# Kernel optimization log

Measured on AMD Instinct MI355X. Metric: run time of the kernel, lower is better.

The kernel has to match this reference:

```python
import jax, jax.numpy as jnp
import numpy as np

GAMMA = 0.95        # gamma_lemma: persistence decay per cycle (eq. 12.1)
KAPPA = 0.1         # kappa_interfere: lateral interference strength (eq. 12.3)
T_STEPS = 50        # t_lemma_steps: integration window before selection (eq. 12.2)
FLOOR = 1e-6        # confidence_floor for peak-to-average ratio

B, N_CONCEPTS, N_LEMMAS = 4096, 1024, 512


def setup_inputs() -> dict:
    key = jax.random.key(0)
    k1, k2 = jax.random.split(key, 2)
    # kernel boundary hands in a normalized concept distribution
    c_raw = jax.random.uniform(k1, (B, N_CONCEPTS), dtype=jnp.float32)
    c_lex = c_raw / jnp.sum(c_raw, axis=-1, keepdims=True)
    # TiedSubstrate W_C_to_L: (out_dim=n_lemmas, in_dim=n_concepts)
    W = jax.random.normal(k2, (N_LEMMAS, N_CONCEPTS), dtype=jnp.float32) / np.sqrt(N_CONCEPTS)
    # persistent lemma activation buffer a_lemma, zero at reset
    a0 = jnp.zeros((B, N_LEMMAS), dtype=jnp.float32)
    return {"c_lex": c_lex, "W": W, "a0": a0}


def reference(c_lex, W, a0):
    """Integrate lemma activations for T_STEPS cycles, then select.

    Per cycle (eq. 12.1 + 12.3):
      a <- gamma * a + c_lex @ W^T            # decay + concept->lemma drive
      a <- a - kappa * (sum_j a_j - a)        # lateral interference from other lemmas
      a <- max(a, 0)                          # rectify activations
    Selection (eq. 12.2): argmax over lemmas; confidence = peak / max(mean, floor).
    """
    def step(a, _):
        a = GAMMA * a + jnp.einsum('bc,lc->bl', c_lex, W)   # (B, n_lemmas)
        a = a - KAPPA * (jnp.sum(a, axis=-1, keepdims=True) - a)
        a = jnp.maximum(a, 0.0)
        return a, None

    a, _ = jax.lax.scan(step, a0, None, length=T_STEPS)
    peak = jnp.max(a, axis=-1)
    mean = jnp.mean(a, axis=-1)
    confidence = peak / jnp.maximum(mean, FLOOR)
    selected = jnp.argmax(a, axis=-1)
    return a, selected, confidence
```

## Files before the change

### kernel.cpp

```cpp
#include <hip/hip_runtime.h>
#include <hip/hip_bf16.h>

#define BATCH 4096
#define NC    1024
#define NL    512
#define TSTEPS 50
#define GAMMA_C 0.95f
#define KAPPA_C 0.1f
#define FLOOR_C 1e-6f

typedef __attribute__((ext_vector_type(8))) short short8;
typedef __attribute__((ext_vector_type(4))) float f32x4;

__device__ __forceinline__ void split2_pk(float x0, float x1,
                                          unsigned& hp, unsigned& lp) {
    union { __hip_bfloat162 b; unsigned u; } ch, cl;
    ch.b = __float22bfloat162_rn(make_float2(x0, x1));
    hp = ch.u;
    const float hf0 = __uint_as_float(hp << 16);
    const float hf1 = __uint_as_float(hp & 0xFFFF0000u);
    cl.b = __float22bfloat162_rn(make_float2(x0 - hf0, x1 - hf1));
    lp = cl.u;
}

#define W_FLOATS (NL * NC)
#define W_BLOCKS (W_FLOATS / (256 * 8))
#define A_BLOCKS ((BATCH * NC) / (256 * 8))

__global__ __launch_bounds__(256)
void convert_hilo(const float* __restrict__ W, const float* __restrict__ A,
                  unsigned short* __restrict__ Whi, unsigned short* __restrict__ Wlo,
                  unsigned short* __restrict__ Ahi, unsigned short* __restrict__ Alo) {
    const int b = blockIdx.x;
    const float* src;
    unsigned short *dh, *dl;
    if (b < W_BLOCKS) {
        const size_t fidx = ((size_t)b * 256 + threadIdx.x) * 8;
        src = W + fidx; dh = Whi + fidx; dl = Wlo + fidx;
    } else {
        const size_t fidx = ((size_t)(b - W_BLOCKS) * 256 + threadIdx.x) * 8;
        src = A + fidx; dh = Ahi + fidx; dl = Alo + fidx;
    }
    const float4 v0 = ((const float4*)src)[0];
    const float4 v1 = ((const float4*)src)[1];
    uint4 h, l;
    split2_pk(v0.x, v0.y, h.x, l.x);
    split2_pk(v0.z, v0.w, h.y, l.y);
    split2_pk(v1.x, v1.y, h.z, l.z);
    split2_pk(v1.z, v1.w, h.w, l.w);
    *(uint4*)dh = h;
    *(uint4*)dl = l;
}

__device__ __forceinline__ float wave_sum_bcast(float x) {
    float f = x;
    f += __int_as_float(__builtin_amdgcn_update_dpp(
            0, __float_as_int(f), 0x111, 0xf, 0xf, true));
    f += __int_as_float(__builtin_amdgcn_update_dpp(
            0, __float_as_int(f), 0x112, 0xf, 0xf, true));
    f += __int_as_float(__builtin_amdgcn_update_dpp(
            0, __float_as_int(f), 0x114, 0xf, 0xf, true));
    f += __int_as_float(__builtin_amdgcn_update_dpp(
            0, __float_as_int(f), 0x118, 0xf, 0xf, true));
    f += __int_as_float(__builtin_amdgcn_update_dpp(
            0, __float_as_int(f), 0x142, 0xa, 0xf, true));
    f += __int_as_float(__builtin_amdgcn_update_dpp(
            0, __float_as_int(f), 0x143, 0xc, 0xf, true));
    return __int_as_float(__builtin_amdgcn_readlane(__float_as_int(f), 63));
}

__device__ __forceinline__ void glds16(const unsigned short* g, unsigned short* l) {
    __builtin_amdgcn_global_load_lds(
        (__attribute__((address_space(1))) void*)(g),
        (__attribute__((address_space(3))) void*)(l), 16, 0, 0);
}

#define TM 128
#define TN 128
#define GK 32
#define SPLITK 4
#define NST (NC / SPLITK / GK)

__global__ __launch_bounds__(256)
void gemm_bf16x2(const unsigned short* __restrict__ Ahi, const unsigned short* __restrict__ Alo,
                 const unsigned short* __restrict__ Whi, const unsigned short* __restrict__ Wlo,
                 float* __restrict__ Dp) {
    __shared__ unsigned short S[2][4][TM * GK];

    const int tid  = threadIdx.x;
    const int lane = tid & 63;
    const int w    = tid >> 6;

    const int b    = blockIdx.x;
    const int xcd  = b & 7;
    const int slot = b >> 3;
    const int mi_b = xcd * 4 + (slot & 3);
    const int nk   = slot >> 2;
    const int ni_b = nk & 3;
    const int kz   = nk >> 2;

    const int m0 = mi_b * TM;
    const int n0 = ni_b * TN;
    const int kb = kz * (NC / SPLITK);

    const int srow = w * 32 + (lane >> 2);
    const int scol = (lane & 3) * 8;
    const unsigned short* gAh = Ahi + (size_t)(m0 + srow) * NC + kb + scol;
    const unsigned short* gAl = Alo + (size_t)(m0 + srow) * NC + kb + scol;
    const unsigned short* gBh = Whi + (size_t)(n0 + srow) * NC + kb + scol;
    const unsigned short* gBl = Wlo + (size_t)(n0 + srow) * NC + kb + scol;
    const int ld0 = (w * 32) * GK + lane * 8;

    const int mw   = (w >> 1) * 64;
    const int nw   = (w & 1) * 64;
    const int sr   = lane & 15;
    const int quad = lane >> 4;
    const int rA = (mw + sr) * GK + quad * 8;
    const int rB = (nw + sr) * GK + quad * 8;

    f32x4 acc[4][4];
    #pragma unroll
    for (int i = 0; i < 4; ++i)
        #pragma unroll
        for (int j = 0; j < 4; ++j)
            acc[i][j] = (f32x4){0.f, 0.f, 0.f, 0.f};

    #define STAGE(buf, kofs)                                          \
        {                                                             \
            const int ko = (kofs);                                    \
            glds16(gAh + ko,           &S[buf][0][ld0]);              \
            glds16(gAh + ko + 16 * NC, &S[buf][0][ld0 + 16 * GK]);    \
            glds16(gAl + ko,           &S[buf][1][ld0]);              \
            glds16(gAl + ko + 16 * NC, &S[buf][1][ld0 + 16 * GK]);    \
            glds16(gBh + ko,           &S[buf][2][ld0]);              \
            glds16(gBh + ko + 16 * NC, &S[buf][2][ld0 + 16 * GK]);    \
            glds16(gBl + ko,           &S[buf][3][ld0]);              \
            glds16(gBl + ko + 16 * NC, &S[buf][3][ld0 + 16 * GK]);    \
        }

    #define KSTEP(CUR, VMSTR, DO_STAGE, NEXTK)                                 \
        {                                                                      \
            asm volatile("s_waitcnt vmcnt(" VMSTR ")" ::: "memory");           \
            __builtin_amdgcn_sched_barrier(0);                                 \
            __builtin_amdgcn_s_barrier();                                      \
            __builtin_amdgcn_sched_barrier(0);                                 \
            short8 afh[4], afl[4], bfh[4], bfl[4];                             \
            _Pragma("unroll")                                                  \
            for (int mi = 0; mi < 4; ++mi) {                                   \
                afh[mi] = *(const short8*)&S[CUR][0][rA + mi * 16 * GK];       \
                afl[mi] = *(const short8*)&S[CUR][1][rA + mi * 16 * GK];       \
            }                                                                  \
            _Pragma("unroll")                                                  \
            for (int ni = 0; ni < 4; ++ni) {                                   \
                bfh[ni] = *(const short8*)&S[CUR][2][rB + ni * 16 * GK];       \
                bfl[ni] = *(const short8*)&S[CUR][3][rB + ni * 16 * GK];       \
            }                                                                  \
            _Pragma("unroll")                                                  \
            for (int mi = 0; mi < 4; ++mi) {                                   \
                _Pragma("unroll")                                              \
                for (int ni = 0; ni < 4; ++ni) {                               \
                    acc[mi][ni] = __builtin_amdgcn_mfma_f32_16x16x32_bf16(     \
                        afh[mi], bfh[ni], acc[mi][ni], 0, 0, 0);               \
                    acc[mi][ni] = __builtin_amdgcn_mfma_f32_16x16x32_bf16(     \
                        afh[mi], bfl[ni], acc[mi][ni], 0, 0, 0);               \
                    acc[mi][ni] = __builtin_amdgcn_mfma_f32_16x16x32_bf16(     \
                        afl[mi], bfh[ni], acc[mi][ni], 0, 0, 0);               \
                }                                                              \
            }                                                                  \
            __builtin_amdgcn_sched_barrier(0);                                 \
            __builtin_amdgcn_s_barrier();                                      \
            __builtin_amdgcn_sched_barrier(0);                                 \
            if (DO_STAGE) STAGE(CUR, NEXTK);                                   \
        }

    STAGE(0, 0);
    STAGE(1, GK);

    #pragma unroll 2
    for (int s = 0; s < NST - 2; ++s)
        KSTEP((s & 1), "8", true, (s + 2) * GK);
    KSTEP(0, "8", false, 0);
    KSTEP(1, "0", false, 0);

    float* Dz = Dp + (size_t)kz * BATCH * NL;
    #pragma unroll
    for (int mi = 0; mi < 4; ++mi) {
        #pragma unroll
        for (int ni = 0; ni < 4; ++ni) {
            const int col = n0 + nw + ni * 16 + sr;
            #pragma unroll
            for (int r = 0; r < 4; ++r) {
                const int row = m0 + mw + mi * 16 + quad * 4 + r;
                Dz[(size_t)row * NL + col] = acc[mi][ni][r];
            }
        }
    }
}

template<int SK>
__global__ __launch_bounds__(256)
void iterate_select(const float* __restrict__ Dp,
                    float* __restrict__ a_out,
                    float* __restrict__ sel_out, float* __restrict__ conf_out) {
    const int lane = threadIdx.x & 63;
    const int wave = threadIdx.x >> 6;
    const int row  = blockIdx.x * 4 + wave;

    float d[8];
    {
        float4 v[SK][2];
        #pragma unroll
        for (int s = 0; s < SK; ++s) {
            const float4* ps = (const float4*)(Dp + (size_t)s * BATCH * NL
                                               + (size_t)row * NL + lane * 8);
            v[s][0] = ps[0];
            v[s][1] = ps[1];
        }
        d[0] = v[0][0].x; d[1] = v[0][0].y; d[2] = v[0][0].z; d[3] = v[0][0].w;
        d[4] = v[0][1].x; d[5] = v[0][1].y; d[6] = v[0][1].z; d[7] = v[0][1].w;
        #pragma unroll
        for (int s = 1; s < SK; ++s) {
            d[0] += v[s][0].x; d[1] += v[s][0].y; d[2] += v[s][0].z; d[3] += v[s][0].w;
            d[4] += v[s][1].x; d[5] += v[s][1].y; d[6] += v[s][1].z; d[7] += v[s][1].w;
        }
    }

    float a[8];
    #pragma unroll
    for (int j = 0; j < 8; ++j) a[j] = 0.f;

    const float K1 = 1.0f + KAPPA_C;

    for (int t = 0; t < TSTEPS; ++t) {
        #pragma unroll
        for (int j = 0; j < 8; ++j) a[j] = fmaf(GAMMA_C, a[j], d[j]);

        float t4a = a[0] + a[4], t4b = a[1] + a[5], t4c = a[2] + a[6], t4d = a[3] + a[7];
        float t2a = t4a + t4c, t2b = t4b + t4d;
        const float S = wave_sum_bcast(t2a + t2b);

        const float h = -KAPPA_C * S;
        #pragma unroll
        for (int j = 0; j < 8; ++j) {
            const float v = fmaf(K1, a[j], h);
            a[j] = v > 0.f ? v : 0.f;
        }
    }

    float m4a = fmaxf(a[0], a[4]), m4b = fmaxf(a[1], a[5]);
    float m4c = fmaxf(a[2], a[6]), m4d = fmaxf(a[3], a[7]);
    float peak = fmaxf(fmaxf(m4a, m4b), fmaxf(m4c, m4d));
    float s4a = a[0] + a[4], s4b = a[1] + a[5], s4c = a[2] + a[6], s4d = a[3] + a[7];
    float ssum = wave_sum_bcast((s4a + s4b) + (s4c + s4d));

    #pragma unroll
    for (int m = 1; m < 64; m <<= 1)
        peak = fmaxf(peak, __shfl_xor(peak, m, 64));

    const float mean = ssum * (1.0f / (float)NL);
    const float conf = peak / fmaxf(mean, FLOOR_C);

    int idx = 0x7fffffff;
    #pragma unroll
    for (int j = 0; j < 8; ++j)
        if (a[j] == peak) idx = min(idx, lane * 8 + j);
    #pragma unroll
    for (int m = 1; m < 64; m <<= 1)
        idx = min(idx, __shfl_xor(idx, m, 64));

    float4* ar = (float4*)(a_out + (size_t)row * NL + lane * 8);
    float4 o0, o1;
    o0.x = a[0]; o0.y = a[1]; o0.z = a[2]; o0.w = a[3];
    o1.x = a[4]; o1.y = a[5]; o1.z = a[6]; o1.w = a[7];
    ar[0] = o0; ar[1] = o1;

    if (lane == 0) {
        if (sel_out)  sel_out[row]  = (float)idx;
        if (conf_out) conf_out[row] = conf;
    }
}

extern "C" void kernel_launch(void* const* d_in, const int* in_sizes, int n_in,
                              void* d_out, int out_size, void* d_ws, size_t ws_size,
                              hipStream_t stream) {
    const float* c_lex = (const float*)d_in[0];
    const float* W     = (const float*)d_in[1];

    float* D = (float*)d_ws;
    unsigned short* Whi = (unsigned short*)(D + (size_t)SPLITK * BATCH * NL);
    unsigned short* Wlo = Whi + (size_t)NL * NC;
    unsigned short* Ahi = Wlo + (size_t)NL * NC;
    unsigned short* Alo = Ahi + (size_t)BATCH * NC;

    float* a_out = (float*)d_out;
    float* sel   = nullptr;
    float* conf  = nullptr;
    const int base = BATCH * NL;
    if (out_size >= base + 2 * BATCH) {
        sel  = a_out + base;
        conf = a_out + base + BATCH;
    } else if (out_size >= base + BATCH) {
        conf = a_out + base;
    }

    convert_hilo<<<dim3(W_BLOCKS + A_BLOCKS), 256, 0, stream>>>(
        W, c_lex, Whi, Wlo, Ahi, Alo);

    gemm_bf16x2<<<dim3(512), 256, 0, stream>>>(Ahi, Alo, Whi, Wlo, D);

    iterate_select<SPLITK><<<dim3(BATCH / 4), 256, 0, stream>>>(D, a_out, sel, conf);
}
```

Measured before the change: 107.7 us.

## Fuse bf16 hi/lo split into GEMM, staging fp32 tiles with swizzled LDS

Removes the separate convert_hilo kernel and its hi/lo bf16 buffers in workspace. The GEMM now loads fp32 tiles of c_lex and W straight into LDS with an XOR swizzle and does the bf16 hi/lo split on the fly while building fragments. This drops one kernel launch and a full read/write pass over A and W. In exchange each block repeats the split arithmetic, and the fp32 staging moves the same bytes through LDS as the old four bf16 arrays.

Measured after the change: 107.9 us. No clear change (+0.2%).

```diff
diff --git a/kernel.cpp b/kernel.cpp
--- a/kernel.cpp
+++ b/kernel.cpp
@@ -23,35 +23,6 @@
     lp = cl.u;
 }
 
-#define W_FLOATS (NL * NC)
-#define W_BLOCKS (W_FLOATS / (256 * 8))
-#define A_BLOCKS ((BATCH * NC) / (256 * 8))
-
-__global__ __launch_bounds__(256)
-void convert_hilo(const float* __restrict__ W, const float* __restrict__ A,
-                  unsigned short* __restrict__ Whi, unsigned short* __restrict__ Wlo,
-                  unsigned short* __restrict__ Ahi, unsigned short* __restrict__ Alo) {
-    const int b = blockIdx.x;
-    const float* src;
-    unsigned short *dh, *dl;
-    if (b < W_BLOCKS) {
-        const size_t fidx = ((size_t)b * 256 + threadIdx.x) * 8;
-        src = W + fidx; dh = Whi + fidx; dl = Wlo + fidx;
-    } else {
-        const size_t fidx = ((size_t)(b - W_BLOCKS) * 256 + threadIdx.x) * 8;
-        src = A + fidx; dh = Ahi + fidx; dl = Alo + fidx;
-    }
-    const float4 v0 = ((const float4*)src)[0];
-    const float4 v1 = ((const float4*)src)[1];
-    uint4 h, l;
-    split2_pk(v0.x, v0.y, h.x, l.x);
-    split2_pk(v0.z, v0.w, h.y, l.y);
-    split2_pk(v1.x, v1.y, h.z, l.z);
-    split2_pk(v1.z, v1.w, h.w, l.w);
-    *(uint4*)dh = h;
-    *(uint4*)dl = l;
-}
-
 __device__ __forceinline__ float wave_sum_bcast(float x) {
     float f = x;
     f += __int_as_float(__builtin_amdgcn_update_dpp(
@@ -69,7 +40,7 @@
     return __int_as_float(__builtin_amdgcn_readlane(__float_as_int(f), 63));
 }
 
-__device__ __forceinline__ void glds16(const unsigned short* g, unsigned short* l) {
+__device__ __forceinline__ void glds16f(const float* g, float* l) {
     __builtin_amdgcn_global_load_lds(
         (__attribute__((address_space(1))) void*)(g),
         (__attribute__((address_space(3))) void*)(l), 16, 0, 0);
@@ -82,10 +53,9 @@
 #define NST (NC / SPLITK / GK)
 
 __global__ __launch_bounds__(256)
-void gemm_bf16x2(const unsigned short* __restrict__ Ahi, const unsigned short* __restrict__ Alo,
-                 const unsigned short* __restrict__ Whi, const unsigned short* __restrict__ Wlo,
-                 float* __restrict__ Dp) {
-    __shared__ unsigned short S[2][4][TM * GK];
+void gemm_f32stage(const float* __restrict__ A, const float* __restrict__ W,
+                   float* __restrict__ Dp) {
+    __shared__ float S[2][2][TM * GK];
 
     const int tid  = threadIdx.x;
     const int lane = tid & 63;
@@ -103,20 +73,21 @@
     const int n0 = ni_b * TN;
     const int kb = kz * (NC / SPLITK);
 
-    const int srow = w * 32 + (lane >> 2);
-    const int scol = (lane & 3) * 8;
-    const unsigned short* gAh = Ahi + (size_t)(m0 + srow) * NC + kb + scol;
-    const unsigned short* gAl = Alo + (size_t)(m0 + srow) * NC + kb + scol;
-    const unsigned short* gBh = Whi + (size_t)(n0 + srow) * NC + kb + scol;
-    const unsigned short* gBl = Wlo + (size_t)(n0 + srow) * NC + kb + scol;
-    const int ld0 = (w * 32) * GK + lane * 8;
+    const int srow = lane >> 3;
+    const int scol = ((lane & 7) * 4) ^ ((srow & 7) << 2);
+    const float* gA = A + (size_t)(m0 + w * 32 + srow) * NC + kb + scol;
+    const float* gB = W + (size_t)(n0 + w * 32 + srow) * NC + kb + scol;
+    const int ldd = (w * 32) * GK;
 
     const int mw   = (w >> 1) * 64;
     const int nw   = (w & 1) * 64;
     const int sr   = lane & 15;
     const int quad = lane >> 4;
-    const int rA = (mw + sr) * GK + quad * 8;
-    const int rB = (nw + sr) * GK + quad * 8;
+    const int swz = (sr & 7) << 2;
+    const int c0  = (quad * 8) ^ swz;
+    const int c1  = (quad * 8 + 4) ^ swz;
+    const int rAo = (mw + sr) * GK;
+    const int rBo = (nw + sr) * GK;
 
     f32x4 acc[4][4];
     #pragma unroll
@@ -125,36 +96,45 @@
         for (int j = 0; j < 4; ++j)
             acc[i][j] = (f32x4){0.f, 0.f, 0.f, 0.f};
 
-    #define STAGE(buf, kofs)                                          \
-        {                                                             \
-            const int ko = (kofs);                                    \
-            glds16(gAh + ko,           &S[buf][0][ld0]);              \
-            glds16(gAh + ko + 16 * NC, &S[buf][0][ld0 + 16 * GK]);    \
-            glds16(gAl + ko,           &S[buf][1][ld0]);              \
-            glds16(gAl + ko + 16 * NC, &S[buf][1][ld0 + 16 * GK]);    \
-            glds16(gBh + ko,           &S[buf][2][ld0]);              \
-            glds16(gBh + ko + 16 * NC, &S[buf][2][ld0 + 16 * GK]);    \
-            glds16(gBl + ko,           &S[buf][3][ld0]);              \
-            glds16(gBl + ko + 16 * NC, &S[buf][3][ld0 + 16 * GK]);    \
-        }
-
-    #define KSTEP(CUR, VMSTR, DO_STAGE, NEXTK)                                 \
+    #define STAGE(buf, kofs)                                               \
+        {                                                                  \
+            const int ko = (kofs);                                         \
+            _Pragma("unroll")                                              \
+            for (int c = 0; c < 4; ++c) {                                  \
+                glds16f(gA + (size_t)(c * 8) * NC + ko,                    \
+                        &S[buf][0][ldd + c * 8 * GK]);                     \
+                glds16f(gB + (size_t)(c * 8) * NC + ko,                    \
+                        &S[buf][1][ldd + c * 8 * GK]);                     \
+            }                                                              \
+        }
+
+    #define FRAG(ARR, ROFF, FH, FL)                                        \
+        {                                                                  \
+            const float4 f0 = *(const float4*)&S[CUR][ARR][(ROFF) + c0];   \
+            const float4 f1 = *(const float4*)&S[CUR][ARR][(ROFF) + c1];   \
+            uint4 hh, ll;                                                  \
+            split2_pk(f0.x, f0.y, hh.x, ll.x);                             \
+            split2_pk(f0.z, f0.w, hh.y, ll.y);                             \
+            split2_pk(f1.x, f1.y, hh.z, ll.z);                             \
+            split2_pk(f1.z, f1.w, hh.w, ll.w);                             \
+            FH = *(const short8*)&hh;                                      \
+            FL = *(const short8*)&ll;                                      \
+        }
+
+    #define KSTEP(CURV, VMSTR, DO_STAGE, NEXTK)                                \
         {                                                                      \
+            const int CUR = (CURV);                                            \
             asm volatile("s_waitcnt vmcnt(" VMSTR ")" ::: "memory");           \
             __builtin_amdgcn_sched_barrier(0);                                 \
             __builtin_amdgcn_s_barrier();                                      \
             __builtin_amdgcn_sched_barrier(0);                                 \
             short8 afh[4], afl[4], bfh[4], bfl[4];                             \
             _Pragma("unroll")                                                  \
-            for (int mi = 0; mi < 4; ++mi) {                                   \
-                afh[mi] = *(const short8*)&S[CUR][0][rA + mi * 16 * GK];       \
-                afl[mi] = *(const short8*)&S[CUR][1][rA + mi * 16 * GK];       \
-            }                                                                  \
+            for (int mi = 0; mi < 4; ++mi)                                     \
+                FRAG(0, rAo + mi * 16 * GK, afh[mi], afl[mi]);                 \
             _Pragma("unroll")                                                  \
-            for (int ni = 0; ni < 4; ++ni) {                                   \
-                bfh[ni] = *(const short8*)&S[CUR][2][rB + ni * 16 * GK];       \
-                bfl[ni] = *(const short8*)&S[CUR][3][rB + ni * 16 * GK];       \
-            }                                                                  \
+            for (int ni = 0; ni < 4; ++ni)                                     \
+                FRAG(1, rBo + ni * 16 * GK, bfh[ni], bfl[ni]);                 \
             _Pragma("unroll")                                                  \
             for (int mi = 0; mi < 4; ++mi) {                                   \
                 _Pragma("unroll")                                              \
@@ -287,10 +267,6 @@
     const float* W     = (const float*)d_in[1];
 
     float* D = (float*)d_ws;
-    unsigned short* Whi = (unsigned short*)(D + (size_t)SPLITK * BATCH * NL);
-    unsigned short* Wlo = Whi + (size_t)NL * NC;
-    unsigned short* Ahi = Wlo + (size_t)NL * NC;
-    unsigned short* Alo = Ahi + (size_t)BATCH * NC;
 
     float* a_out = (float*)d_out;
     float* sel   = nullptr;
@@ -303,10 +279,7 @@
         conf = a_out + base;
     }
 
-    convert_hilo<<<dim3(W_BLOCKS + A_BLOCKS), 256, 0, stream>>>(
-        W, c_lex, Whi, Wlo, Ahi, Alo);
-
-    gemm_bf16x2<<<dim3(512), 256, 0, stream>>>(Ahi, Alo, Whi, Wlo, D);
+    gemm_f32stage<<<dim3(512), 256, 0, stream>>>(c_lex, W, D);
 
     iterate_select<SPLITK><<<dim3(BATCH / 4), 256, 0, stream>>>(D, a_out, sel, conf);
 }
```
